# Kernel optimization log

Measured on AMD Instinct MI355X. Metric: run time of the kernel, lower is better.

The kernel has to match this reference:

```python
import jax, jax.numpy as jnp
import numpy as np

B, S, V = 2048, 200, 50257
E, H, EMB = 60, 30, 20  # encode_size, hidden_size, embed_size


def setup_inputs() -> dict:
    key = jax.random.key(0)
    ks = jax.random.split(key, 24)
    emb = jax.random.normal(ks[7], (V, EMB), jnp.float32) * 0.02
    emb = emb.at[3].set(0.0)  # padding_idx=3
    inp = {
        'coverage': jax.random.uniform(ks[0], (B, S), jnp.float32),
        'enc_out': jax.random.normal(ks[1], (B, S, E), jnp.float32),
        'h0': jax.random.normal(ks[2], (1, B, H), jnp.float32),
        'c0': jax.random.normal(ks[3], (1, B, H), jnp.float32),
        'attn': jax.random.uniform(ks[4], (B, S), jnp.float32),
        'dec_input': jax.random.randint(ks[5], (B, 1), 0, V, jnp.int32),
        'enc_inputs': jax.random.randint(ks[6], (B, S), 0, V, jnp.int32),
        'embedding': emb,
        # LSTM (torch gate order i,f,g,o)
        'w_ih': jax.random.normal(ks[8], (4 * H, EMB + E), jnp.float32) * 0.1,
        'w_hh': jax.random.normal(ks[9], (4 * H, H), jnp.float32) * 0.1,
        'b_ih': jax.random.normal(ks[10], (4 * H,), jnp.float32) * 0.1,
        'b_hh': jax.random.normal(ks[11], (4 * H,), jnp.float32) * 0.1,
        # Attention submodule
        'attn_wh_w': jax.random.normal(ks[12], (H, E), jnp.float32) * 0.1,
        'attn_wh_b': jax.random.normal(ks[13], (H,), jnp.float32) * 0.1,
        'attn_ws_w': jax.random.normal(ks[14], (H, H), jnp.float32) * 0.1,
        'attn_ws_b': jax.random.normal(ks[15], (H,), jnp.float32) * 0.1,
        'attn_wc': jax.random.uniform(ks[16], (H,), jnp.float32),
        'attn_v': jax.random.uniform(ks[17], (H,), jnp.float32),
        # pointer-gen params
        'wh': jax.random.uniform(ks[18], (E,), jnp.float32),
        'ws': jax.random.uniform(ks[19], (H,), jnp.float32),
        'wx': jax.random.uniform(ks[20], (EMB,), jnp.float32),
        'v_w': jax.random.normal(ks[21], (V, H), jnp.float32) * 0.02,
        'v_b': jax.random.normal(ks[22], (V,), jnp.float32) * 0.02,
    }
    return inp


def reference(coverage, enc_out, h0, c0, attn, dec_input, enc_inputs, embedding,
              w_ih, w_hh, b_ih, b_hh, attn_wh_w, attn_wh_b, attn_ws_w, attn_ws_b,
              attn_wc, attn_v, wh, ws, wx, v_w, v_b):
    # context = bmm(attn[B,1,S], enc_out[B,S,E]) -> [B,E]
    context = jnp.einsum('bs,bse->be', attn, enc_out)
    embed = embedding[dec_input[:, 0]]              # [B,EMB]
    x = jnp.concatenate([context, embed], axis=-1)  # [B,E+EMB]
    # single-step LSTM (torch gate order i,f,g,o)
    gates = x @ w_ih.T + b_ih + h0[0] @ w_hh.T + b_hh
    i, f, g, o = jnp.split(gates, 4, axis=-1)
    c = jax.nn.sigmoid(f) * c0[0] + jax.nn.sigmoid(i) * jnp.tanh(g)
    h = jax.nn.sigmoid(o) * jnp.tanh(c)             # rnn_out [B,H]
    p_vocab = jax.nn.softmax(h @ v_w.T + v_b, axis=1)   # [B,V]
    p_gen = jax.nn.sigmoid(context @ wh + h @ ws + embed @ wx)[:, None]  # [B,1]
    # attention
    wh_app = enc_out @ attn_wh_w.T + attn_wh_b      # [B,S,H]
    ws_app = (h @ attn_ws_w.T + attn_ws_b)[:, None, :]  # [B,1,H]
    wc_app = coverage[..., None] * attn_wc          # [B,S,H]
    energy = jnp.tanh(wh_app + ws_app + wc_app) @ attn_v  # [B,S]
    new_attn = jax.nn.softmax(energy, axis=1)
    coverage_loss = jnp.sum(jnp.minimum(new_attn, coverage))
    new_coverage = coverage + new_attn
    # scatter copy-attention into vocab space (duplicate idx: arbitrary winner, as torch scatter_)
    rows = jnp.arange(enc_inputs.shape[0])[:, None]
    attn_scores = jnp.zeros((enc_inputs.shape[0], v_w.shape[0]), p_vocab.dtype).at[rows, enc_inputs].set(new_attn)
    output = p_gen * p_vocab + (1.0 - p_gen) * attn_scores
    return output, new_coverage, (h[None], c[None]), new_attn, coverage_loss
```

## Files before the change

### kernel.cpp

```cpp
#include <hip/hip_runtime.h>

#define BB 2048
#define SS 200
#define VV 50257
#define EE 60
#define HH 30
#define EMBD 20
#define XD 80
#define G4 120
#define NCHUNK 50
#define VPAD 51200
#define SROW 68

#define O_COV ((size_t)BB*VV)
#define O_H   (O_COV + (size_t)BB*SS)
#define O_C   (O_H + (size_t)BB*HH)
#define O_NA  (O_C + (size_t)BB*HH)
#define O_LOSS (O_NA + (size_t)BB*SS)

typedef __attribute__((ext_vector_type(8))) short short8v;
typedef __attribute__((ext_vector_type(4))) float f32x4;

__device__ __forceinline__ float sigf(float x){ return 1.f/(1.f+__expf(-x)); }

__device__ __forceinline__ short f2bf(float f){
  union { __bf16 h; short s; } u; u.h = (__bf16)f; return u.s;
}

__device__ __forceinline__ float bsum(float v, float* red, int tid){
  #pragma unroll
  for (int off=32; off; off>>=1) v += __shfl_xor(v, off);
  __syncthreads();
  if ((tid&63)==0) red[tid>>6]=v;
  __syncthreads();
  return red[0]+red[1]+red[2]+red[3];
}
__device__ __forceinline__ float bmax(float v, float* red, int tid){
  #pragma unroll
  for (int off=32; off; off>>=1) v = fmaxf(v, __shfl_xor(v, off));
  __syncthreads();
  if ((tid&63)==0) red[tid>>6]=v;
  __syncthreads();
  return fmaxf(fmaxf(red[0],red[1]),fmaxf(red[2],red[3]));
}

__global__ __launch_bounds__(256) void k_pack(
  const float* __restrict__ v_w, const float* __restrict__ v_b,
  short* __restrict__ vw_bf, float* __restrict__ vb_pad)
{
  const int idx = blockIdx.x*256 + threadIdx.x;
  const int col = idx>>2, q = idx&3;
  union { short8v v; short s[8]; } u;
  #pragma unroll
  for (int j=0;j<8;j++){
    int k = q*8+j;
    u.s[j] = (col<VV && k<HH) ? f2bf(v_w[(size_t)col*HH+k]) : (short)0;
  }
  ((short8v*)vw_bf)[idx] = u.v;
  if (q==0) vb_pad[col] = (col<VV) ? v_b[col] : -1e30f;
}

__global__ __launch_bounds__(256) void k_row(
  const float* __restrict__ coverage, const float* __restrict__ enc_out,
  const float* __restrict__ h0, const float* __restrict__ c0,
  const float* __restrict__ attn, const int* __restrict__ dec_input,
  const float* __restrict__ embedding,
  const float* __restrict__ w_ih, const float* __restrict__ w_hh,
  const float* __restrict__ b_ih, const float* __restrict__ b_hh,
  const float* __restrict__ attn_wh_w, const float* __restrict__ attn_wh_b,
  const float* __restrict__ attn_ws_w, const float* __restrict__ attn_ws_b,
  const float* __restrict__ attn_wc, const float* __restrict__ attn_v,
  const float* __restrict__ whv, const float* __restrict__ wsv, const float* __restrict__ wxv,
  float* __restrict__ out, float* __restrict__ pgen_ws,
  float* __restrict__ losspart_ws, short* __restrict__ h_bf)
{
  const int b = blockIdx.x, tid = threadIdx.x;
  __shared__ float enc[SS*61];
  __shared__ float wT[EE*32];
  __shared__ float attn_s[SS], cov_s[SS];
  __shared__ float xls[XD], hls[HH], wsapp[HH], wc_s[HH], v_s[HH], gls[G4];
  __shared__ float ctxp[EE*4];
  __shared__ float red[4];

  {
    const float4* ep = (const float4*)(enc_out + (size_t)b*(SS*EE));
    #pragma unroll
    for (int it=0; it<12; ++it){
      int i = tid + it*256;
      if (i < (SS*EE/4)) {
        float4 v = ep[i];
        int s = i/15, e4 = (i - s*15)*4;
        float* d = &enc[s*61+e4];
        d[0]=v.x; d[1]=v.y; d[2]=v.z; d[3]=v.w;
      }
    }
  }
  if (tid < SS) { attn_s[tid]=attn[(size_t)b*SS+tid]; cov_s[tid]=coverage[(size_t)b*SS+tid]; }
  for (int i=tid; i<EE*HH; i+=256){ int h=i/EE, e=i-h*EE; wT[e*32+h]=attn_wh_w[i]; }
  if (tid >= 256-HH) { int h = tid-(256-HH); wc_s[h]=attn_wc[h]; v_s[h]=attn_v[h]; }
  __syncthreads();

  if (tid < 240){
    int g = tid/60, e = tid - g*60;
    float acc=0.f;
    for (int s=g; s<SS; s+=4) acc += attn_s[s]*enc[s*61+e];
    ctxp[e*4+g]=acc;
  }
  __syncthreads();
  if (tid < EE) xls[tid]=ctxp[tid*4]+ctxp[tid*4+1]+ctxp[tid*4+2]+ctxp[tid*4+3];
  else if (tid < EE+EMBD){
    int k = tid-EE;
    int dix = dec_input[b];
    xls[tid] = embedding[(size_t)dix*EMBD+k];
  }
  __syncthreads();

  if (tid < G4){
    float acc = b_ih[tid]+b_hh[tid];
    const float* wi = w_ih + tid*XD;
    #pragma unroll
    for (int k=0;k<XD;k++) acc += xls[k]*wi[k];
    const float* whh = w_hh + tid*HH;
    const float* h0b = h0 + (size_t)b*HH;
    #pragma unroll
    for (int k=0;k<HH;k++) acc += h0b[k]*whh[k];
    gls[tid]=acc;
  }
  __syncthreads();
  if (tid < HH){
    float c = sigf(gls[tid+HH])*c0[(size_t)b*HH+tid] + sigf(gls[tid])*tanhf(gls[tid+2*HH]);
    float h = sigf(gls[tid+3*HH])*tanhf(c);
    out[O_C+(size_t)b*HH+tid]=c;
    out[O_H+(size_t)b*HH+tid]=h;
    hls[tid]=h;
  }
  __syncthreads();
  if (tid < 4){
    union { short8v v; short s[8]; } u;
    #pragma unroll
    for (int j=0;j<8;j++){ int k=tid*8+j; u.s[j] = (k<HH)? f2bf(hls[k]) : (short)0; }
    ((short8v*)(h_bf + (size_t)b*32))[tid] = u.v;
  }
  if (tid < HH){
    float acc = attn_ws_b[tid] + attn_wh_b[tid];
    const float* w = attn_ws_w + tid*HH;
    #pragma unroll
    for (int k=0;k<HH;k++) acc += hls[k]*w[k];
    wsapp[tid]=acc;
  }
  float pv=0.f;
  if (tid<EE) pv = xls[tid]*whv[tid];
  else if (tid<EE+HH) pv = hls[tid-EE]*wsv[tid-EE];
  else if (tid<EE+HH+EMBD) pv = xls[EE+(tid-EE-HH)]*wxv[tid-EE-HH];
  float pg = sigf(bsum(pv,red,tid));
  if (tid==0) pgen_ws[b]=pg;
  __syncthreads();

  float en = -1e30f;
  if (tid < SS){
    float acc[HH];
    float cv = cov_s[tid];
    #pragma unroll
    for (int h=0;h<HH;h++) acc[h] = wsapp[h] + cv*wc_s[h];
    for (int e=0;e<EE;e++){
      float evv = enc[tid*61+e];
      #pragma unroll
      for (int h=0;h<HH;h++) acc[h] += evv*wT[e*32+h];
    }
    float e2=0.f;
    #pragma unroll
    for (int h=0;h<HH;h++) e2 += tanhf(acc[h])*v_s[h];
    en = e2;
  }
  float mx = bmax(en, red, tid);
  float ex = (tid<SS)? __expf(en-mx) : 0.f;
  float sm = bsum(ex, red, tid);
  float inv = 1.f/sm;
  float lossv = 0.f;
  if (tid<SS){
    float na = ex*inv;
    float cv = cov_s[tid];
    out[O_NA+(size_t)b*SS+tid]=na;
    out[O_COV+(size_t)b*SS+tid]=cv+na;
    lossv = fminf(na,cv);
  }
  float ls = bsum(lossv,red,tid);
  if (tid==0) losspart_ws[b]=ls;
}

__global__ __launch_bounds__(256) void k_vsum(
  const short* __restrict__ vw_bf, const float* __restrict__ vb_pad,
  const short* __restrict__ h_bf, float* __restrict__ partial)
{
  const int tid = threadIdx.x;
  const int w = tid>>6, l = tid&63;
  const int lc = l&15, lg = l>>4;
  const int task = blockIdx.x*4 + w;
  const int rg = task & 127, cg = task >> 7;
  const int rbase = rg*16, cbase = cg*1024;

  short8v Af = *(const short8v*)(h_bf + (size_t)(rbase+lc)*32 + lg*8);

  float psum[4] = {0.f,0.f,0.f,0.f};
  #pragma unroll 4
  for (int t=0;t<64;t++){
    const int col = cbase + t*16 + lc;
    short8v Bf = *(const short8v*)(vw_bf + (size_t)col*32 + lg*8);
    const float vb = vb_pad[col];
    f32x4 z = {0.f,0.f,0.f,0.f};
    f32x4 d = __builtin_amdgcn_mfma_f32_16x16x32_bf16(Af, Bf, z, 0,0,0);
    psum[0] += __expf(d[0]+vb);
    psum[1] += __expf(d[1]+vb);
    psum[2] += __expf(d[2]+vb);
    psum[3] += __expf(d[3]+vb);
  }
  #pragma unroll
  for (int r=0;r<4;r++){
    float s = psum[r];
    s += __shfl_xor(s,1); s += __shfl_xor(s,2); s += __shfl_xor(s,4); s += __shfl_xor(s,8);
    if (lc==0) partial[(size_t)cg*BB + rbase + lg*4 + r] = s;
  }
}

__global__ __launch_bounds__(256) void k_off(
  const float* __restrict__ partial, const float* __restrict__ pgen,
  float* __restrict__ offs)
{
  const int row = blockIdx.x*256 + threadIdx.x;
  float s=0.f;
  #pragma unroll 5
  for (int c=0;c<NCHUNK;c++) s += partial[(size_t)c*BB + row];
  offs[row] = __logf(pgen[row]) - __logf(s);
}

__global__ __launch_bounds__(256) void k_vwrite(
  const short* __restrict__ vw_bf, const float* __restrict__ vb_pad,
  const short* __restrict__ h_bf, const float* __restrict__ offs,
  float* __restrict__ out)
{
  __shared__ short h_lds[16*32];
  __shared__ float stage[4][16*SROW];
  const int tid = threadIdx.x;
  const int rbase = blockIdx.y*16;
  const int cbase = blockIdx.x*2048;
  if (tid < 64) ((uint4*)h_lds)[tid] = ((const uint4*)(h_bf + (size_t)rbase*32))[tid];
  __syncthreads();

  const int w = tid>>6, l = tid&63;
  const int lc = l&15, lg = l>>4;

  short8v Af = *(const short8v*)&h_lds[lc*32 + lg*8];
  float offv[4];
  #pragma unroll
  for (int r=0;r<4;r++) offv[r] = offs[rbase + lg*4 + r];

  float* sw = stage[w];
  const int wc0 = cbase + w*512;

  for (int c=0;c<8;c++){
    const int c0 = wc0 + c*64;
    #pragma unroll
    for (int t=0;t<4;t++){
      const int col = c0 + t*16 + lc;
      short8v Bf = *(const short8v*)(vw_bf + (size_t)col*32 + lg*8);
      const float vb = vb_pad[col];
      f32x4 z = {0.f,0.f,0.f,0.f};
      f32x4 d = __builtin_amdgcn_mfma_f32_16x16x32_bf16(Af, Bf, z, 0,0,0);
      #pragma unroll
      for (int r=0;r<4;r++)
        sw[(lg*4+r)*SROW + t*16 + lc] = __expf(d[r]+vb+offv[r]);
    }
    #pragma unroll 4
    for (int i=0;i<16;i++){
      if (c0 + l < VV)
        out[(size_t)(rbase+i)*VV + c0 + l] = sw[i*SROW + l];
    }
  }
}

__global__ __launch_bounds__(256) void k_scatter(
  const int* __restrict__ enc_inputs, const float* __restrict__ pgen,
  const float* __restrict__ na, float* __restrict__ out)
{
  __shared__ int idx_s[SS];
  const int b=blockIdx.x, tid=threadIdx.x;
  if (tid<SS) idx_s[tid]=enc_inputs[(size_t)b*SS+tid];
  __syncthreads();
  if (tid<SS){
    int idx=idx_s[tid];
    bool last=true;
    for (int s2=tid+1;s2<SS;s2++) if (idx_s[s2]==idx){ last=false; break; }
    if (last){
      float add=(1.f-pgen[b])*na[(size_t)b*SS+tid];
      out[(size_t)b*VV+idx]+=add;
    }
  }
}

__global__ __launch_bounds__(256) void k_loss(const float* __restrict__ lp, float* __restrict__ dst){
  __shared__ float red[4];
  int tid=threadIdx.x;
  float s=0.f;
  for (int i=tid;i<BB;i+=256) s+=lp[i];
  #pragma unroll
  for (int off=32; off; off>>=1) s+=__shfl_xor(s,off);
  if ((tid&63)==0) red[tid>>6]=s;
  __syncthreads();
  if (tid==0) dst[0]=red[0]+red[1]+red[2]+red[3];
}

extern "C" void kernel_launch(void* const* d_in, const int* in_sizes, int n_in,
                              void* d_out, int out_size, void* d_ws, size_t ws_size,
                              hipStream_t stream)
{
  const float* coverage =(const float*)d_in[0];
  const float* enc_out  =(const float*)d_in[1];
  const float* h0       =(const float*)d_in[2];
  const float* c0       =(const float*)d_in[3];
  const float* attn     =(const float*)d_in[4];
  const int*   dec_input=(const int*)d_in[5];
  const int*   enc_inputs=(const int*)d_in[6];
  const float* embedding=(const float*)d_in[7];
  const float* w_ih     =(const float*)d_in[8];
  const float* w_hh     =(const float*)d_in[9];
  const float* b_ih     =(const float*)d_in[10];
  const float* b_hh     =(const float*)d_in[11];
  const float* attn_wh_w=(const float*)d_in[12];
  const float* attn_wh_b=(const float*)d_in[13];
  const float* attn_ws_w=(const float*)d_in[14];
  const float* attn_ws_b=(const float*)d_in[15];
  const float* attn_wc  =(const float*)d_in[16];
  const float* attn_v   =(const float*)d_in[17];
  const float* whv      =(const float*)d_in[18];
  const float* wsv      =(const float*)d_in[19];
  const float* wxv      =(const float*)d_in[20];
  const float* v_w      =(const float*)d_in[21];
  const float* v_b      =(const float*)d_in[22];
  float* out=(float*)d_out;
  float* wsf=(float*)d_ws;
  float* pgen    = wsf;
  float* losspart= wsf + 2048;
  float* offs    = wsf + 4096;
  float* partial = wsf + 6144;
  float* vb_pad  = wsf + 6144 + (size_t)NCHUNK*BB;
  short* vw_bf   = (short*)(vb_pad + VPAD);
  short* h_bf    = vw_bf + (size_t)VPAD*32;

  k_pack<<<VPAD*4/256,256,0,stream>>>(v_w,v_b,vw_bf,vb_pad);

  k_row<<<BB,256,0,stream>>>(coverage,enc_out,h0,c0,attn,dec_input,embedding,
    w_ih,w_hh,b_ih,b_hh,attn_wh_w,attn_wh_b,attn_ws_w,attn_ws_b,attn_wc,attn_v,
    whv,wsv,wxv,out,pgen,losspart,h_bf);

  k_vsum  <<<1600,256,0,stream>>>(vw_bf,vb_pad,h_bf,partial);
  k_off   <<<BB/256,256,0,stream>>>(partial,pgen,offs);
  dim3 gw(VPAD/2048, BB/16);
  k_vwrite<<<gw,256,0,stream>>>(vw_bf,vb_pad,h_bf,offs,out);
  k_scatter<<<BB,256,0,stream>>>(enc_inputs,pgen,out+O_NA,out);
  k_loss<<<1,256,0,stream>>>(losspart,out+O_LOSS);
}
```

Baseline: 346.3 us.

## Swap MFMA operands so each lane writes contiguous vocab columns directly

Swaps the A/B operands of the bf16 MFMA so the vocab dimension lands on the accumulator row axis and each lane holds four consecutive columns of one batch row. k_vwrite drops its LDS staging buffer and sync and writes 16-byte vector stores straight to the output, with a scalar tail at the vocab edge. Work is remapped to a 1D grid of 1024 blocks covering 1600 columns per wave. k_vsum uses the same orientation with vectorized bias loads and a shorter cross-lane reduction. The risk is that each lane's 16-byte stores go to a different row, so a wave's writes are spread over 16 rows rather than coalesced along one row.

After: 343.6 us. About the same (-0.8%).

```diff
diff --git a/kernel.cpp b/kernel.cpp
--- a/kernel.cpp
+++ b/kernel.cpp
@@ -10,7 +10,6 @@
 #define G4 120
 #define NCHUNK 50
 #define VPAD 51200
-#define SROW 68
 
 #define O_COV ((size_t)BB*VV)
 #define O_H   (O_COV + (size_t)BB*SS)
@@ -20,6 +19,7 @@
 
 typedef __attribute__((ext_vector_type(8))) short short8v;
 typedef __attribute__((ext_vector_type(4))) float f32x4;
+typedef __attribute__((ext_vector_type(4), aligned(4))) float f32x4u;
 
 __device__ __forceinline__ float sigf(float x){ return 1.f/(1.f+__expf(-x)); }
 
@@ -199,27 +199,22 @@
   const int rg = task & 127, cg = task >> 7;
   const int rbase = rg*16, cbase = cg*1024;
 
-  short8v Af = *(const short8v*)(h_bf + (size_t)(rbase+lc)*32 + lg*8);
-
-  float psum[4] = {0.f,0.f,0.f,0.f};
+  short8v Bh = *(const short8v*)(h_bf + (size_t)(rbase+lc)*32 + lg*8);
+
+  float ps = 0.f;
   #pragma unroll 4
   for (int t=0;t<64;t++){
-    const int col = cbase + t*16 + lc;
-    short8v Bf = *(const short8v*)(vw_bf + (size_t)col*32 + lg*8);
-    const float vb = vb_pad[col];
+    const int ct = cbase + t*16;
+    short8v Av = *(const short8v*)(vw_bf + (size_t)(ct+lc)*32 + lg*8);
+    f32x4 vb4 = *(const f32x4*)(vb_pad + ct + lg*4);
     f32x4 z = {0.f,0.f,0.f,0.f};
-    f32x4 d = __builtin_amdgcn_mfma_f32_16x16x32_bf16(Af, Bf, z, 0,0,0);
-    psum[0] += __expf(d[0]+vb);
-    psum[1] += __expf(d[1]+vb);
-    psum[2] += __expf(d[2]+vb);
-    psum[3] += __expf(d[3]+vb);
-  }
-  #pragma unroll
-  for (int r=0;r<4;r++){
-    float s = psum[r];
-    s += __shfl_xor(s,1); s += __shfl_xor(s,2); s += __shfl_xor(s,4); s += __shfl_xor(s,8);
-    if (lc==0) partial[(size_t)cg*BB + rbase + lg*4 + r] = s;
-  }
+    f32x4 d = __builtin_amdgcn_mfma_f32_16x16x32_bf16(Av, Bh, z, 0,0,0);
+    ps += __expf(d[0]+vb4[0]) + __expf(d[1]+vb4[1])
+        + __expf(d[2]+vb4[2]) + __expf(d[3]+vb4[3]);
+  }
+  ps += __shfl_xor(ps,16);
+  ps += __shfl_xor(ps,32);
+  if (l < 16) partial[(size_t)cg*BB + rbase + lc] = ps;
 }
 
 __global__ __launch_bounds__(256) void k_off(
@@ -238,42 +233,36 @@
   const short* __restrict__ h_bf, const float* __restrict__ offs,
   float* __restrict__ out)
 {
-  __shared__ short h_lds[16*32];
-  __shared__ float stage[4][16*SROW];
   const int tid = threadIdx.x;
-  const int rbase = blockIdx.y*16;
-  const int cbase = blockIdx.x*2048;
-  if (tid < 64) ((uint4*)h_lds)[tid] = ((const uint4*)(h_bf + (size_t)rbase*32))[tid];
-  __syncthreads();
-
   const int w = tid>>6, l = tid&63;
   const int lc = l&15, lg = l>>4;
-
-  short8v Af = *(const short8v*)&h_lds[lc*32 + lg*8];
-  float offv[4];
-  #pragma unroll
-  for (int r=0;r<4;r++) offv[r] = offs[rbase + lg*4 + r];
-
-  float* sw = stage[w];
-  const int wc0 = cbase + w*512;
-
-  for (int c=0;c<8;c++){
-    const int c0 = wc0 + c*64;
-    #pragma unroll
-    for (int t=0;t<4;t++){
-      const int col = c0 + t*16 + lc;
-      short8v Bf = *(const short8v*)(vw_bf + (size_t)col*32 + lg*8);
-      const float vb = vb_pad[col];
-      f32x4 z = {0.f,0.f,0.f,0.f};
-      f32x4 d = __builtin_amdgcn_mfma_f32_16x16x32_bf16(Af, Bf, z, 0,0,0);
+  const int task = blockIdx.x*4 + w;
+  const int rg = task & 127, cg = task >> 7;
+  const int rbase = rg*16, cbase = cg*1600;
+
+  short8v Bh = *(const short8v*)(h_bf + (size_t)(rbase+lc)*32 + lg*8);
+  const int row = rbase + lc;
+  const float off = offs[row];
+  float* orow = out + (size_t)row*VV;
+
+  #pragma unroll 2
+  for (int t=0;t<100;t++){
+    const int ct = cbase + t*16;
+    const int v0 = ct + lg*4;
+    short8v Av = *(const short8v*)(vw_bf + (size_t)(ct+lc)*32 + lg*8);
+    f32x4 vb4 = *(const f32x4*)(vb_pad + v0);
+    f32x4 z = {0.f,0.f,0.f,0.f};
+    f32x4 d = __builtin_amdgcn_mfma_f32_16x16x32_bf16(Av, Bh, z, 0,0,0);
+    f32x4 o;
+    o[0] = __expf(d[0]+vb4[0]+off);
+    o[1] = __expf(d[1]+vb4[1]+off);
+    o[2] = __expf(d[2]+vb4[2]+off);
+    o[3] = __expf(d[3]+vb4[3]+off);
+    if (v0 + 4 <= VV){
+      *(f32x4u*)(orow + v0) = o;
+    } else {
       #pragma unroll
-      for (int r=0;r<4;r++)
-        sw[(lg*4+r)*SROW + t*16 + lc] = __expf(d[r]+vb+offv[r]);
-    }
-    #pragma unroll 4
-    for (int i=0;i<16;i++){
-      if (c0 + l < VV)
-        out[(size_t)(rbase+i)*VV + c0 + l] = sw[i*SROW + l];
+      for (int r=0;r<4;r++) if (v0 + r < VV) orow[v0+r] = o[r];
     }
   }
 }
@@ -354,8 +343,7 @@
 
   k_vsum  <<<1600,256,0,stream>>>(vw_bf,vb_pad,h_bf,partial);
   k_off   <<<BB/256,256,0,stream>>>(partial,pgen,offs);
-  dim3 gw(VPAD/2048, BB/16);
-  k_vwrite<<<gw,256,0,stream>>>(vw_bf,vb_pad,h_bf,offs,out);
+  k_vwrite<<<1024,256,0,stream>>>(vw_bf,vb_pad,h_bf,offs,out);
   k_scatter<<<BB,256,0,stream>>>(enc_inputs,pgen,out+O_NA,out);
   k_loss<<<1,256,0,stream>>>(losspart,out+O_LOSS);
 }
```
